# Performance work log

Measured on AMD Instinct MI355X. Metric: run time of the kernel, lower is better.

The kernel has to match this reference:

```python
import jax, jax.numpy as jnp
import numpy as np
from jax import lax

NEG = jnp.float32(-1e9)
POS = jnp.float32(1e9)


def _edt_sq(mask):
    """Exact squared Euclidean distance transform of a 2D boolean mask.

    mask: [H, W] bool, True = foreground (nonzero in scipy terms).
    Returns [H, W] float32 squared distance to nearest background (False) pixel.
    Felzenszwalb-Huttenlocher separable formulation:
      pass 1 (axis 0): 1D distance to nearest zero per column (O(H) via scans)
      pass 2 (axis 1): min-plus convolution with quadratic per row.
    """
    H, W = mask.shape
    zero = ~mask
    idx = jnp.broadcast_to(jnp.arange(H, dtype=jnp.float32)[:, None], (H, W))
    # index of last background pixel at-or-above, and next at-or-below, per column
    last0 = lax.associative_scan(jnp.maximum, jnp.where(zero, idx, NEG), axis=0)
    next0 = jnp.flip(
        lax.associative_scan(jnp.minimum, jnp.flip(jnp.where(zero, idx, POS), 0), axis=0), 0)
    d1 = jnp.minimum(idx - last0, next0 - idx)  # 1D distance along axis 0
    f = jnp.where(mask, d1 * d1, jnp.float32(0.0))  # squared axis-0 distance
    # pass 2: D[i, j] = min_j' f[i, j'] + (j - j')^2
    jq = jnp.arange(W, dtype=jnp.float32)
    q = (jq[:, None] - jq[None, :]) ** 2  # [W, W]
    def row_min(frow):  # frow: [W]
        return jnp.min(frow[None, :] + q, axis=1)  # [W]
    return lax.map(row_min, f)  # [H, W]


def setup_inputs() -> dict:
    key = jax.random.key(0)
    img = jax.random.uniform(key, (2048, 2048), dtype=jnp.float32)
    return {"img": img}


def reference(img) -> jnp.ndarray:
    mask = img > 0.5  # scipy: nonzero pixels are foreground
    d = jnp.sqrt(_edt_sq(mask))
    m = jnp.max(d)
    d = jnp.where(m > 0, d / m * 255.0, d)  # `if img.max() != 0: img = img/max*255`
    return d.astype(jnp.uint8)  # img.astype(np.uint8)
```

## Files before the change

### kernel.cpp

```cpp
#include <hip/hip_runtime.h>
#include <math.h>

typedef unsigned long long u64;

#define H 2048
#define W 2048
#define NWR 64
#define TILE 128
#define HALO 32
#define LW 192
#define LSTRIDE 193
#define DCLAMP 2900
#define NTHR 256
#define NBLK 1024

#define TAG_V  0x33C0FFEEull
#define TAG_F  0x44C0FFEEull

__device__ __attribute__((noinline)) int vfar_up_img(const float* img, int col, int r, int rtop) {
    for (int rr = rtop - 1; rr >= 0; --rr)
        if (img[(size_t)rr * W + col] <= 0.5f) return r - rr;
    return DCLAMP;
}
__device__ __attribute__((noinline)) int vfar_dn_img(const float* img, int col, int r, int rbot) {
    for (int rr = rbot + 1; rr < H; ++rr)
        if (img[(size_t)rr * W + col] <= 0.5f) return rr - r;
    return DCLAMP;
}
__device__ __attribute__((noinline)) float f_from_img(const float* img, int col, int r) {
    if (img[(size_t)r * W + col] <= 0.5f) return 0.0f;
    int du = DCLAMP, dn = DCLAMP;
    for (int dd = 1; r - dd >= 0; ++dd)
        if (img[(size_t)(r - dd) * W + col] <= 0.5f) { du = dd; break; }
    for (int dd = 1; r + dd < H; ++dd)
        if (img[(size_t)(r + dd) * W + col] <= 0.5f) { dn = dd; break; }
    int d1 = min(min(du, dn), DCLAMP);
    return (float)d1 * (float)d1;
}

__global__ void __launch_bounds__(NTHR, 4)
edt_solo(const float* __restrict__ img, int* __restrict__ out,
         u64* __restrict__ vcell, u64* __restrict__ flag) {
    __shared__ float ftile[32][LSTRIDE];
    __shared__ float smax[5];
    const int tid = threadIdx.x;
    const int c0 = blockIdx.x * TILE;
    const int ks = blockIdx.y;
    const int rbase = ks * 32;
    const int bid = ks * (W / TILE) + blockIdx.x;

    if (tid < LW) {
        int gc = c0 - HALO + tid;
        if (gc >= 0 && gc < W) {
            unsigned wm1 = 0, w0 = 0, wp1 = 0;
            if (ks > 0) {
#pragma unroll
                for (int i = 0; i < 32; ++i)
                    wm1 |= (img[(size_t)(rbase - 32 + i) * W + gc] <= 0.5f ? 1u : 0u) << i;
            }
#pragma unroll
            for (int i = 0; i < 32; ++i)
                w0 |= (img[(size_t)(rbase + i) * W + gc] <= 0.5f ? 1u : 0u) << i;
            if (ks < NWR - 1) {
#pragma unroll
                for (int i = 0; i < 32; ++i)
                    wp1 |= (img[(size_t)(rbase + 32 + i) * W + gc] <= 0.5f ? 1u : 0u) << i;
            }
            u64 A  = (u64)wm1 | ((u64)w0 << 32);
            u64 Bv = (u64)w0  | ((u64)wp1 << 32);
#pragma unroll
            for (int i = 0; i < 32; ++i) {
                int p = 32 + i;
                u64 Am = A & ((1ull << p) - 1ull);
                int da = Am ? (p - (63 - __clzll(Am)))
                            : vfar_up_img(img, gc, rbase + i, rbase - 32);
                u64 Bm = Bv >> (i + 1);
                int db = Bm ? __ffsll(Bm)
                            : vfar_dn_img(img, gc, rbase + i, rbase + 63);
                int d1 = min(min(da, db), DCLAMP);
                float fd = (float)d1;
                ftile[i][tid] = ((w0 >> i) & 1u) ? 0.0f : fd * fd;
            }
        } else {
#pragma unroll
            for (int i = 0; i < 32; ++i)
                ftile[i][tid] = 1e9f;
        }
    }
    __syncthreads();

    const int i  = tid & 31;
    const int p  = tid >> 5;
    const int lc = HALO + p * 16;
    float reg[32];
#pragma unroll
    for (int k = 0; k < 32; ++k)
        reg[k] = ftile[i][lc - 8 + k];

    float res[16];
    float lmax = 0.0f;
#pragma unroll
    for (int m = 0; m < 16; ++m) {
        float best = reg[m + 8];
#pragma unroll
        for (int d = 1; d <= 8; ++d) {
            float q = (float)(d * d);
            best = fminf(best, reg[m + 8 - d] + q);
            best = fminf(best, reg[m + 8 + d] + q);
        }
        if (__builtin_expect(81.0f < best, 0)) {
            for (int d = 9; d <= HALO && (float)(d * d) < best; ++d) {
                float q = (float)(d * d);
                best = fminf(best, ftile[i][lc + m - d] + q);
                best = fminf(best, ftile[i][lc + m + d] + q);
            }
            if ((float)((HALO + 1) * (HALO + 1)) < best) {
                int r = rbase + i, jj = c0 + p * 16 + m;
                for (int d = HALO + 1; d < W && (float)(d * d) < best; ++d) {
                    float q = (float)(d * d);
                    int jm = jj - d, jp = jj + d;
                    if (jm >= 0) best = fminf(best, f_from_img(img, jm, r) + q);
                    if (jp < W)  best = fminf(best, f_from_img(img, jp, r) + q);
                }
            }
        }
        float rr = sqrtf(best);
        res[m] = rr;
        lmax = fmaxf(lmax, rr);
    }

    __syncthreads();
#pragma unroll
    for (int m = 0; m < 16; ++m)
        ftile[i][p * 16 + m] = res[m];

    for (int o = 32; o > 0; o >>= 1) lmax = fmaxf(lmax, __shfl_down(lmax, o, 64));
    if ((tid & 63) == 0) smax[1 + (tid >> 6)] = lmax;
    __syncthreads();

    if (tid == 0) {
        float bm = fmaxf(fmaxf(smax[1], smax[2]), fmaxf(smax[3], smax[4]));
        u64 v = (TAG_V << 32) | (u64)__float_as_uint(bm);
        __hip_atomic_store(&vcell[bid], v, __ATOMIC_RELAXED, __HIP_MEMORY_SCOPE_AGENT);
    }
    if (bid == 0) {
        float mv = 0.0f;
#pragma unroll
        for (int k = 0; k < NBLK / NTHR; ++k) {
            u64 v;
            while (((v = __hip_atomic_load(&vcell[tid * (NBLK / NTHR) + k],
                                           __ATOMIC_RELAXED, __HIP_MEMORY_SCOPE_AGENT))
                    >> 32) != TAG_V)
                __builtin_amdgcn_s_sleep(2);
            mv = fmaxf(mv, __uint_as_float((unsigned)v));
        }
        for (int o = 32; o > 0; o >>= 1) mv = fmaxf(mv, __shfl_down(mv, o, 64));
        if ((tid & 63) == 0) smax[1 + (tid >> 6)] = mv;
        __syncthreads();
        if (tid == 0) {
            float gm = fmaxf(fmaxf(smax[1], smax[2]), fmaxf(smax[3], smax[4]));
            smax[0] = gm;
            u64 v = (TAG_F << 32) | (u64)__float_as_uint(gm);
            __hip_atomic_store(flag, v, __ATOMIC_RELAXED, __HIP_MEMORY_SCOPE_AGENT);
        }
    } else if (tid == 0) {
        u64 v;
        while (((v = __hip_atomic_load(flag, __ATOMIC_RELAXED,
                                       __HIP_MEMORY_SCOPE_AGENT)) >> 32) != TAG_F)
            __builtin_amdgcn_s_sleep(8);
        smax[0] = __uint_as_float((unsigned)v);
    }
    __syncthreads();

    float m = smax[0];
    float scale = (m > 0.0f) ? 1.0f / m : 0.0f;
#pragma unroll
    for (int q = 0; q < 4; ++q) {
        int r  = (tid >> 5) + 8 * q;
        int c4 = (tid & 31) * 4;
        int o[4];
#pragma unroll
        for (int k = 0; k < 4; ++k) {
            float dv = ftile[r][c4 + k];
            float v = (m > 0.0f) ? (dv * scale * 255.0f) : dv;
            v = fminf(fmaxf(v, 0.0f), 255.0f);
            o[k] = (int)v;
        }
        *(int4*)(out + (size_t)(rbase + r) * W + c0 + c4) = make_int4(o[0], o[1], o[2], o[3]);
    }
}

extern "C" void kernel_launch(void* const* d_in, const int* in_sizes, int n_in,
                              void* d_out, int out_size, void* d_ws, size_t ws_size,
                              hipStream_t stream) {
    const float* img = (const float*)d_in[0];
    int* out = (int*)d_out;

    u64* vcell = (u64*)d_ws;
    u64* flag  = (u64*)((char*)d_ws + 8192 + 128);

    edt_solo<<<dim3(W / TILE, NWR), dim3(NTHR), 0, stream>>>(img, out, vcell, flag);
}
```

Baseline: 81.30 us.

## Widen column tiles to halve blocks and shard the global-max broadcast flag

Doubles the tile width to 256 columns so each block processes two 16-column strips per thread. That cuts the block count from 1024 to 512 and shrinks the relative halo overhead (64 halo columns per 256 instead of per 128). The broadcast of the global max is spread across 32 flag slots on separate cache lines, so waiting blocks poll different addresses instead of all spinning on one. In exchange each block does more serial work, uses more LDS, and has a lower occupancy hint, which may reduce latency hiding.

```diff
diff --git a/kernel.cpp b/kernel.cpp
--- a/kernel.cpp
+++ b/kernel.cpp
@@ -6,13 +6,14 @@
 #define H 2048
 #define W 2048
 #define NWR 64
-#define TILE 128
+#define TILE 256
 #define HALO 32
-#define LW 192
-#define LSTRIDE 193
+#define LW 320
+#define LSTRIDE 321
 #define DCLAMP 2900
 #define NTHR 256
-#define NBLK 1024
+#define NBLK 512
+#define NSHARD 32
 
 #define TAG_V  0x33C0FFEEull
 #define TAG_F  0x44C0FFEEull
@@ -38,9 +39,49 @@
     return (float)d1 * (float)d1;
 }
 
-__global__ void __launch_bounds__(NTHR, 4)
+__device__ __forceinline__ void pack_decode_col(const float* __restrict__ img,
+                                                float (*ftile)[LSTRIDE],
+                                                int lc, int gc, int ks, int rbase) {
+    if (gc >= 0 && gc < W) {
+        unsigned wm1 = 0, w0 = 0, wp1 = 0;
+        if (ks > 0) {
+#pragma unroll
+            for (int i = 0; i < 32; ++i)
+                wm1 |= (img[(size_t)(rbase - 32 + i) * W + gc] <= 0.5f ? 1u : 0u) << i;
+        }
+#pragma unroll
+        for (int i = 0; i < 32; ++i)
+            w0 |= (img[(size_t)(rbase + i) * W + gc] <= 0.5f ? 1u : 0u) << i;
+        if (ks < NWR - 1) {
+#pragma unroll
+            for (int i = 0; i < 32; ++i)
+                wp1 |= (img[(size_t)(rbase + 32 + i) * W + gc] <= 0.5f ? 1u : 0u) << i;
+        }
+        u64 A  = (u64)wm1 | ((u64)w0 << 32);
+        u64 Bv = (u64)w0  | ((u64)wp1 << 32);
+#pragma unroll
+        for (int i = 0; i < 32; ++i) {
+            int p = 32 + i;
+            u64 Am = A & ((1ull << p) - 1ull);
+            int da = Am ? (p - (63 - __clzll(Am)))
+                        : vfar_up_img(img, gc, rbase + i, rbase - 32);
+            u64 Bm = Bv >> (i + 1);
+            int db = Bm ? __ffsll(Bm)
+                        : vfar_dn_img(img, gc, rbase + i, rbase + 63);
+            int d1 = min(min(da, db), DCLAMP);
+            float fd = (float)d1;
+            ftile[i][lc] = ((w0 >> i) & 1u) ? 0.0f : fd * fd;
+        }
+    } else {
+#pragma unroll
+        for (int i = 0; i < 32; ++i)
+            ftile[i][lc] = 1e9f;
+    }
+}
+
+__global__ void __launch_bounds__(NTHR, 3)
 edt_solo(const float* __restrict__ img, int* __restrict__ out,
-         u64* __restrict__ vcell, u64* __restrict__ flag) {
+         u64* __restrict__ vcell, u64* __restrict__ flags) {
     __shared__ float ftile[32][LSTRIDE];
     __shared__ float smax[5];
     const int tid = threadIdx.x;
@@ -49,91 +90,60 @@
     const int rbase = ks * 32;
     const int bid = ks * (W / TILE) + blockIdx.x;
 
-    if (tid < LW) {
-        int gc = c0 - HALO + tid;
-        if (gc >= 0 && gc < W) {
-            unsigned wm1 = 0, w0 = 0, wp1 = 0;
-            if (ks > 0) {
-#pragma unroll
-                for (int i = 0; i < 32; ++i)
-                    wm1 |= (img[(size_t)(rbase - 32 + i) * W + gc] <= 0.5f ? 1u : 0u) << i;
+    pack_decode_col(img, ftile, tid, c0 - HALO + tid, ks, rbase);
+    if (tid < LW - NTHR)
+        pack_decode_col(img, ftile, NTHR + tid, c0 - HALO + NTHR + tid, ks, rbase);
+    __syncthreads();
+
+    const int i = tid & 31;
+    const int p0 = tid >> 5;
+    float res[2][16];
+    float lmax = 0.0f;
+#pragma unroll
+    for (int sp = 0; sp < 2; ++sp) {
+        const int p  = p0 + sp * 8;
+        const int lc = HALO + p * 16;
+        float reg[32];
+#pragma unroll
+        for (int k = 0; k < 32; ++k)
+            reg[k] = ftile[i][lc - 8 + k];
+#pragma unroll
+        for (int m = 0; m < 16; ++m) {
+            float best = reg[m + 8];
+#pragma unroll
+            for (int d = 1; d <= 8; ++d) {
+                float q = (float)(d * d);
+                best = fminf(best, reg[m + 8 - d] + q);
+                best = fminf(best, reg[m + 8 + d] + q);
             }
-#pragma unroll
-            for (int i = 0; i < 32; ++i)
-                w0 |= (img[(size_t)(rbase + i) * W + gc] <= 0.5f ? 1u : 0u) << i;
-            if (ks < NWR - 1) {
-#pragma unroll
-                for (int i = 0; i < 32; ++i)
-                    wp1 |= (img[(size_t)(rbase + 32 + i) * W + gc] <= 0.5f ? 1u : 0u) << i;
-            }
-            u64 A  = (u64)wm1 | ((u64)w0 << 32);
-            u64 Bv = (u64)w0  | ((u64)wp1 << 32);
-#pragma unroll
-            for (int i = 0; i < 32; ++i) {
-                int p = 32 + i;
-                u64 Am = A & ((1ull << p) - 1ull);
-                int da = Am ? (p - (63 - __clzll(Am)))
-                            : vfar_up_img(img, gc, rbase + i, rbase - 32);
-                u64 Bm = Bv >> (i + 1);
-                int db = Bm ? __ffsll(Bm)
-                            : vfar_dn_img(img, gc, rbase + i, rbase + 63);
-                int d1 = min(min(da, db), DCLAMP);
-                float fd = (float)d1;
-                ftile[i][tid] = ((w0 >> i) & 1u) ? 0.0f : fd * fd;
-            }
-        } else {
-#pragma unroll
-            for (int i = 0; i < 32; ++i)
-                ftile[i][tid] = 1e9f;
-        }
-    }
-    __syncthreads();
-
-    const int i  = tid & 31;
-    const int p  = tid >> 5;
-    const int lc = HALO + p * 16;
-    float reg[32];
-#pragma unroll
-    for (int k = 0; k < 32; ++k)
-        reg[k] = ftile[i][lc - 8 + k];
-
-    float res[16];
-    float lmax = 0.0f;
-#pragma unroll
-    for (int m = 0; m < 16; ++m) {
-        float best = reg[m + 8];
-#pragma unroll
-        for (int d = 1; d <= 8; ++d) {
-            float q = (float)(d * d);
-            best = fminf(best, reg[m + 8 - d] + q);
-            best = fminf(best, reg[m + 8 + d] + q);
-        }
-        if (__builtin_expect(81.0f < best, 0)) {
-            for (int d = 9; d <= HALO && (float)(d * d) < best; ++d) {
-                float q = (float)(d * d);
-                best = fminf(best, ftile[i][lc + m - d] + q);
-                best = fminf(best, ftile[i][lc + m + d] + q);
-            }
-            if ((float)((HALO + 1) * (HALO + 1)) < best) {
-                int r = rbase + i, jj = c0 + p * 16 + m;
-                for (int d = HALO + 1; d < W && (float)(d * d) < best; ++d) {
+            if (__builtin_expect(81.0f < best, 0)) {
+                for (int d = 9; d <= HALO && (float)(d * d) < best; ++d) {
                     float q = (float)(d * d);
-                    int jm = jj - d, jp = jj + d;
-                    if (jm >= 0) best = fminf(best, f_from_img(img, jm, r) + q);
-                    if (jp < W)  best = fminf(best, f_from_img(img, jp, r) + q);
+                    best = fminf(best, ftile[i][lc + m - d] + q);
+                    best = fminf(best, ftile[i][lc + m + d] + q);
+                }
+                if ((float)((HALO + 1) * (HALO + 1)) < best) {
+                    int r = rbase + i, jj = c0 + p * 16 + m;
+                    for (int d = HALO + 1; d < W && (float)(d * d) < best; ++d) {
+                        float q = (float)(d * d);
+                        int jm = jj - d, jp = jj + d;
+                        if (jm >= 0) best = fminf(best, f_from_img(img, jm, r) + q);
+                        if (jp < W)  best = fminf(best, f_from_img(img, jp, r) + q);
+                    }
                 }
             }
-        }
-        float rr = sqrtf(best);
-        res[m] = rr;
-        lmax = fmaxf(lmax, rr);
-    }
-
-    __syncthreads();
-#pragma unroll
-    for (int m = 0; m < 16; ++m)
-        ftile[i][p * 16 + m] = res[m];
-
+            float rr = sqrtf(best);
+            res[sp][m] = rr;
+            lmax = fmaxf(lmax, rr);
+        }
+    }
+
+    __syncthreads();
+#pragma unroll
+    for (int m = 0; m < 16; ++m) {
+        ftile[i][p0 * 16 + m]       = res[0][m];
+        ftile[i][(p0 + 8) * 16 + m] = res[1][m];
+    }
     for (int o = 32; o > 0; o >>= 1) lmax = fmaxf(lmax, __shfl_down(lmax, o, 64));
     if ((tid & 63) == 0) smax[1 + (tid >> 6)] = lmax;
     __syncthreads();
@@ -157,16 +167,18 @@
         for (int o = 32; o > 0; o >>= 1) mv = fmaxf(mv, __shfl_down(mv, o, 64));
         if ((tid & 63) == 0) smax[1 + (tid >> 6)] = mv;
         __syncthreads();
-        if (tid == 0) {
-            float gm = fmaxf(fmaxf(smax[1], smax[2]), fmaxf(smax[3], smax[4]));
-            smax[0] = gm;
-            u64 v = (TAG_F << 32) | (u64)__float_as_uint(gm);
-            __hip_atomic_store(flag, v, __ATOMIC_RELAXED, __HIP_MEMORY_SCOPE_AGENT);
+        if (tid == 0) smax[0] = fmaxf(fmaxf(smax[1], smax[2]), fmaxf(smax[3], smax[4]));
+        __syncthreads();
+        if (tid < NSHARD) {
+            u64 v = (TAG_F << 32) | (u64)__float_as_uint(smax[0]);
+            __hip_atomic_store(&flags[tid * 16], v, __ATOMIC_RELAXED,
+                               __HIP_MEMORY_SCOPE_AGENT);
         }
     } else if (tid == 0) {
         u64 v;
-        while (((v = __hip_atomic_load(flag, __ATOMIC_RELAXED,
-                                       __HIP_MEMORY_SCOPE_AGENT)) >> 32) != TAG_F)
+        while (((v = __hip_atomic_load(&flags[(bid & (NSHARD - 1)) * 16],
+                                       __ATOMIC_RELAXED, __HIP_MEMORY_SCOPE_AGENT))
+                >> 32) != TAG_F)
             __builtin_amdgcn_s_sleep(8);
         smax[0] = __uint_as_float((unsigned)v);
     }
@@ -175,9 +187,10 @@
     float m = smax[0];
     float scale = (m > 0.0f) ? 1.0f / m : 0.0f;
 #pragma unroll
-    for (int q = 0; q < 4; ++q) {
-        int r  = (tid >> 5) + 8 * q;
-        int c4 = (tid & 31) * 4;
+    for (int q = 0; q < 8; ++q) {
+        int n  = q * NTHR + tid;
+        int r  = n >> 6;
+        int c4 = (n & 63) * 4;
         int o[4];
 #pragma unroll
         for (int k = 0; k < 4; ++k) {
@@ -197,7 +210,7 @@
     int* out = (int*)d_out;
 
     u64* vcell = (u64*)d_ws;
-    u64* flag  = (u64*)((char*)d_ws + 8192 + 128);
-
-    edt_solo<<<dim3(W / TILE, NWR), dim3(NTHR), 0, stream>>>(img, out, vcell, flag);
-}
+    u64* flags = (u64*)((char*)d_ws + 4096);
+
+    edt_solo<<<dim3(W / TILE, NWR), dim3(NTHR), 0, stream>>>(img, out, vcell, flags);
+}
```

Result: slower. 85.35 us (+5.0%).
